# Kernel tuning notes

Measured on AMD Instinct MI355X. Metric: run time of the kernel, lower is better.

## Reference

```python
import jax, jax.numpy as jnp
import numpy as np

GAMMA = 0.01
INFER_STEP = 3


def softor(x, axis, gamma=GAMMA):
    # smoothed logic-OR: gamma*logsumexp(x/gamma), normalized if it exceeds 1 (alphailp/NSFR semantics)
    lse = gamma * jax.nn.logsumexp(x / gamma, axis=axis)
    m = jnp.max(lse)
    return jnp.where(m > 1.0, lse / m, lse)


def clause_eval(R, I, gamma=GAMMA):
    # R: [C,B,G] per-clause valuations, I: [C,G,S,L] index tensor (values in [0,G))
    # gathered[c,b,g,s,l] = R[c, b, I[c,g,s,l]]
    gathered = jax.vmap(lambda Rc, Ic: jnp.take(Rc, Ic, axis=1))(R, I)  # [C,B,G,S,L]
    body = jnp.prod(gathered, axis=-1)  # product over body atoms L -> [C,B,G,S]
    return softor(body, axis=-1, gamma=gamma)  # soft-OR over substitutions S -> [C,B,G]


def setup_inputs() -> dict:
    key = jax.random.key(0)
    k1, k2 = jax.random.split(key)
    C, B, G, S, L = 4, 128, 2048, 32, 3
    x = jax.random.uniform(k1, (B, G), dtype=jnp.float32)  # atom valuations in [0,1]
    I = jax.random.randint(k2, (C, G, S, L), 0, G, dtype=jnp.int32)
    return {"x": x, "I": I}


def reference(x, I):
    C = I.shape[0]
    B, G = x.shape
    R = jnp.broadcast_to(x[None], (C, B, G))  # expand to per-clause valuation
    for _ in range(INFER_STEP):
        # amalgamate previous valuation with one inference step via soft-OR along stacked dim
        R = softor(jnp.stack([R, clause_eval(R, I)], axis=1), axis=1)
    return R
```

## Files before the change

### kernel.cpp

```cpp
#include <hip/hip_runtime.h>
#include <cstdint>
#include <cstddef>

#define C_ 4
#define B_ 128
#define G_ 2048
#define S_ 32
#define L_ 3
#define NSTEP_ 3
#define GAMMA_ 0.01f
#define INVG_LOG2E_ 144.26950408889634f
#define GAMMA_LN2_ 0.0069314718055994530942f

__device__ __forceinline__ float slot_max(const uint32_t* slots, int slot) {
  float m = 0.0f;
#pragma unroll
  for (int k = 0; k < 8; ++k)
    m = fmaxf(m, __uint_as_float(slots[slot * 128 + k * 16]));
  return m;
}

__global__ __launch_bounds__(256) void k_init(const float* __restrict__ x,
                                              float* __restrict__ A) {
  __shared__ float tile[32][33];
  const int g0 = blockIdx.x * 32, b0 = blockIdx.y * 32, c = blockIdx.z;
  const int tx = threadIdx.x;
  for (int i = threadIdx.y; i < 32; i += 8)
    tile[i][tx] = x[(size_t)(b0 + i) * G_ + g0 + tx];
  __syncthreads();
  for (int j = threadIdx.y; j < 32; j += 8)
    A[((size_t)c * G_ + g0 + j) * B_ + b0 + tx] = tile[tx][j];
}

__global__ __launch_bounds__(128) void k_gather(const float* __restrict__ A,
                                                const int* __restrict__ Idx,
                                                float* __restrict__ Lout,
                                                uint32_t* slots,
                                                int prev_slot, int out_slot) {
  __shared__ int sidx[S_ * L_];
  __shared__ float wmax[2];
  const int tid = threadIdx.x;
  const int bid = blockIdx.x;
  const int cg = ((bid & 7) << 10) | (bid >> 3);
  const int c = cg >> 11;

  if (tid < S_ * L_) sidx[tid] = Idx[(size_t)cg * (S_ * L_) + tid];
  const float mprev = slot_max(slots, prev_slot);
  const float scale = (mprev > 1.0f) ? (1.0f / mprev) : 1.0f;
  const float s3 = scale * scale * scale;
  __syncthreads();

  const float* Ac = A + (size_t)c * (G_ * B_) + tid;
  float body[S_];
#pragma unroll
  for (int s = 0; s < S_; ++s) {
    const float v0 = Ac[(size_t)sidx[3 * s + 0] * B_];
    const float v1 = Ac[(size_t)sidx[3 * s + 1] * B_];
    const float v2 = Ac[(size_t)sidx[3 * s + 2] * B_];
    body[s] = v0 * v1 * v2;
  }
  float m = body[0];
#pragma unroll
  for (int s = 1; s < S_; ++s) m = fmaxf(m, body[s]);
  const float K = s3 * INVG_LOG2E_;
  float acc = 0.0f;
#pragma unroll
  for (int s = 0; s < S_; ++s) acc += exp2f((body[s] - m) * K);
  const float lse = m * s3 + GAMMA_LN2_ * log2f(acc);
  Lout[(size_t)cg * B_ + tid] = lse;

  float t = lse;
#pragma unroll
  for (int off = 32; off >= 1; off >>= 1) t = fmaxf(t, __shfl_xor(t, off));
  if ((tid & 63) == 0) wmax[tid >> 6] = t;
  __syncthreads();
  if (tid == 0)
    atomicMax(slots + out_slot * 128 + (bid & 7) * 16,
              __float_as_uint(fmaxf(wmax[0], wmax[1])));
}

__global__ __launch_bounds__(256) void k_elem(float* __restrict__ A,
                                              const float* __restrict__ Lin,
                                              uint32_t* slots,
                                              int prev_slot, int m1_slot,
                                              int out_slot) {
  __shared__ float wmax[4];
  const float mprev = slot_max(slots, prev_slot);
  const float sprev = (mprev > 1.0f) ? (1.0f / mprev) : 1.0f;
  const float m1 = slot_max(slots, m1_slot);
  const float s1 = (m1 > 1.0f) ? (1.0f / m1) : 1.0f;

  const int e = (blockIdx.x * 256 + threadIdx.x) * 4;
  const float4 Rv = *reinterpret_cast<const float4*>(A + e);
  const float4 Lv = *reinterpret_cast<const float4*>(Lin + e);

  float r[4] = {Rv.x, Rv.y, Rv.z, Rv.w};
  float l[4] = {Lv.x, Lv.y, Lv.z, Lv.w};
  float o[4];
  float tmax = 0.0f;
#pragma unroll
  for (int k = 0; k < 4; ++k) {
    const float R = r[k] * sprev;
    const float ce = l[k] * s1;
    const float M = fmaxf(R, ce);
    const float mn = fminf(R, ce);
    const float lse2 =
        M + GAMMA_LN2_ * log2f(1.0f + exp2f((mn - M) * INVG_LOG2E_));
    o[k] = lse2;
    tmax = fmaxf(tmax, lse2);
  }
  *reinterpret_cast<float4*>(A + e) = make_float4(o[0], o[1], o[2], o[3]);

  float t = tmax;
#pragma unroll
  for (int off = 32; off >= 1; off >>= 1) t = fmaxf(t, __shfl_xor(t, off));
  if ((threadIdx.x & 63) == 0) wmax[threadIdx.x >> 6] = t;
  __syncthreads();
  if (threadIdx.x == 0) {
    const float bm =
        fmaxf(fmaxf(wmax[0], wmax[1]), fmaxf(wmax[2], wmax[3]));
    atomicMax(slots + out_slot * 128 + (blockIdx.x & 7) * 16,
              __float_as_uint(bm));
  }
}

__global__ __launch_bounds__(256) void k_out(const float* __restrict__ A,
                                             float* __restrict__ out,
                                             const uint32_t* __restrict__ slots,
                                             int mslot) {
  __shared__ float tile[32][33];
  const float mfin = slot_max(slots, mslot);
  const float sc = (mfin > 1.0f) ? (1.0f / mfin) : 1.0f;
  const int g0 = blockIdx.x * 32, b0 = blockIdx.y * 32, c = blockIdx.z;
  const int tx = threadIdx.x;
  for (int j = threadIdx.y; j < 32; j += 8)
    tile[j][tx] = A[((size_t)c * G_ + g0 + j) * B_ + b0 + tx];
  __syncthreads();
  for (int i = threadIdx.y; i < 32; i += 8)
    out[((size_t)c * B_ + b0 + i) * G_ + g0 + tx] = tile[tx][i] * sc;
}

extern "C" void kernel_launch(void* const* d_in, const int* in_sizes, int n_in,
                              void* d_out, int out_size, void* d_ws,
                              size_t ws_size, hipStream_t stream) {
  const float* x = (const float*)d_in[0];
  const int* Idx = (const int*)d_in[1];
  float* out = (float*)d_out;

  char* ws = (char*)d_ws;
  uint32_t* slots = (uint32_t*)ws;
  float* A = (float*)(ws + 4096);
  float* Lb = (float*)(ws + 4096 + (size_t)C_ * G_ * B_ * 4);

  hipMemsetAsync(slots, 0, 4096, stream);

  dim3 tb(32, 8);
  k_init<<<dim3(G_ / 32, B_ / 32, C_), tb, 0, stream>>>(x, A);

  for (int step = 0; step < NSTEP_; ++step) {
    const int prev = 2 * step;
    const int m1s = 2 * step + 1;
    const int m2s = 2 * step + 2;
    k_gather<<<C_ * G_, 128, 0, stream>>>(A, Idx, Lb, slots, prev, m1s);
    k_elem<<<(C_ * G_ * B_) / (256 * 4), 256, 0, stream>>>(A, Lb, slots, prev,
                                                           m1s, m2s);
  }

  k_out<<<dim3(G_ / 32, B_ / 32, C_), tb, 0, stream>>>(A, out, slots,
                                                       2 * NSTEP_);
}
```

Measured before the change: 163.2 us.

## Use single-wave gather with online logsumexp and shared transposed input for first step

The gather kernel now runs one 64-lane wave per (clause, atom) row. Each lane handles two batch elements with float2 loads and reads indices through readfirstlane scalar loads, dropping the shared-memory staging and the block barrier. The 32-element body array is replaced by an online max/logsumexp recurrence, which trades register pressure for extra exp2 work. The init kernel also writes one transposed copy of x instead of four per-clause copies, and step 0 reads that copy with a zero clause stride, cutting init writes and improving cache hits on the first gather.

Result: slower. 243.9 us (+49.4%).

```diff
diff --git a/kernel.cpp b/kernel.cpp
--- a/kernel.cpp
+++ b/kernel.cpp
@@ -20,70 +20,69 @@
   return m;
 }
 
-__global__ __launch_bounds__(256) void k_init(const float* __restrict__ x,
-                                              float* __restrict__ A) {
+__global__ __launch_bounds__(256) void k_initT(const float* __restrict__ x,
+                                               float* __restrict__ xT) {
   __shared__ float tile[32][33];
-  const int g0 = blockIdx.x * 32, b0 = blockIdx.y * 32, c = blockIdx.z;
+  const int g0 = blockIdx.x * 32, b0 = blockIdx.y * 32;
   const int tx = threadIdx.x;
   for (int i = threadIdx.y; i < 32; i += 8)
     tile[i][tx] = x[(size_t)(b0 + i) * G_ + g0 + tx];
   __syncthreads();
   for (int j = threadIdx.y; j < 32; j += 8)
-    A[((size_t)c * G_ + g0 + j) * B_ + b0 + tx] = tile[tx][j];
+    xT[(size_t)(g0 + j) * B_ + b0 + tx] = tile[tx][j];
 }
 
-__global__ __launch_bounds__(128) void k_gather(const float* __restrict__ A,
-                                                const int* __restrict__ Idx,
-                                                float* __restrict__ Lout,
-                                                uint32_t* slots,
-                                                int prev_slot, int out_slot) {
-  __shared__ int sidx[S_ * L_];
-  __shared__ float wmax[2];
-  const int tid = threadIdx.x;
+__global__ __launch_bounds__(64, 4) void k_gather(
+    const float* __restrict__ Abase, size_t cstride,
+    const int* __restrict__ Idx, float* __restrict__ Lout,
+    uint32_t* slots, int prev_slot, int out_slot) {
+  const int lane = threadIdx.x;
   const int bid = blockIdx.x;
   const int cg = ((bid & 7) << 10) | (bid >> 3);
   const int c = cg >> 11;
 
-  if (tid < S_ * L_) sidx[tid] = Idx[(size_t)cg * (S_ * L_) + tid];
   const float mprev = slot_max(slots, prev_slot);
   const float scale = (mprev > 1.0f) ? (1.0f / mprev) : 1.0f;
   const float s3 = scale * scale * scale;
-  __syncthreads();
+  const float K = s3 * INVG_LOG2E_;
 
-  const float* Ac = A + (size_t)c * (G_ * B_) + tid;
-  float body[S_];
+  const int ibase = cg * (S_ * L_);
+  const float* Ac = Abase + (size_t)c * cstride + 2 * lane;
+
+  float M0 = -1.0f, M1 = -1.0f;
+  float acc0 = 0.0f, acc1 = 0.0f;
 #pragma unroll
   for (int s = 0; s < S_; ++s) {
-    const float v0 = Ac[(size_t)sidx[3 * s + 0] * B_];
-    const float v1 = Ac[(size_t)sidx[3 * s + 1] * B_];
-    const float v2 = Ac[(size_t)sidx[3 * s + 2] * B_];
-    body[s] = v0 * v1 * v2;
+    const int r0 = __builtin_amdgcn_readfirstlane(Idx[ibase + 3 * s + 0]);
+    const int r1 = __builtin_amdgcn_readfirstlane(Idx[ibase + 3 * s + 1]);
+    const int r2 = __builtin_amdgcn_readfirstlane(Idx[ibase + 3 * s + 2]);
+    const float2 v0 = *(const float2*)(Ac + (size_t)r0 * B_);
+    const float2 v1 = *(const float2*)(Ac + (size_t)r1 * B_);
+    const float2 v2 = *(const float2*)(Ac + (size_t)r2 * B_);
+    const float b0 = v0.x * v1.x * v2.x;
+    const float b1 = v0.y * v1.y * v2.y;
+    const float n0 = fmaxf(M0, b0);
+    acc0 = acc0 * exp2f((M0 - n0) * K) + exp2f((b0 - n0) * K);
+    M0 = n0;
+    const float n1 = fmaxf(M1, b1);
+    acc1 = acc1 * exp2f((M1 - n1) * K) + exp2f((b1 - n1) * K);
+    M1 = n1;
   }
-  float m = body[0];
-#pragma unroll
-  for (int s = 1; s < S_; ++s) m = fmaxf(m, body[s]);
-  const float K = s3 * INVG_LOG2E_;
-  float acc = 0.0f;
-#pragma unroll
-  for (int s = 0; s < S_; ++s) acc += exp2f((body[s] - m) * K);
-  const float lse = m * s3 + GAMMA_LN2_ * log2f(acc);
-  Lout[(size_t)cg * B_ + tid] = lse;
+  const float lse0 = M0 * s3 + GAMMA_LN2_ * log2f(acc0);
+  const float lse1 = M1 * s3 + GAMMA_LN2_ * log2f(acc1);
+  *(float2*)(Lout + (size_t)cg * B_ + 2 * lane) = make_float2(lse0, lse1);
 
-  float t = lse;
+  float t = fmaxf(lse0, lse1);
 #pragma unroll
   for (int off = 32; off >= 1; off >>= 1) t = fmaxf(t, __shfl_xor(t, off));
-  if ((tid & 63) == 0) wmax[tid >> 6] = t;
-  __syncthreads();
-  if (tid == 0)
-    atomicMax(slots + out_slot * 128 + (bid & 7) * 16,
-              __float_as_uint(fmaxf(wmax[0], wmax[1])));
+  if (lane == 0)
+    atomicMax(slots + out_slot * 128 + (bid & 7) * 16, __float_as_uint(t));
 }
 
-__global__ __launch_bounds__(256) void k_elem(float* __restrict__ A,
-                                              const float* __restrict__ Lin,
-                                              uint32_t* slots,
-                                              int prev_slot, int m1_slot,
-                                              int out_slot) {
+__global__ __launch_bounds__(256) void k_elem(
+    const float* __restrict__ Rin, size_t rstride, float* __restrict__ A,
+    const float* __restrict__ Lin, uint32_t* slots, int prev_slot,
+    int m1_slot, int out_slot) {
   __shared__ float wmax[4];
   const float mprev = slot_max(slots, prev_slot);
   const float sprev = (mprev > 1.0f) ? (1.0f / mprev) : 1.0f;
@@ -91,7 +90,9 @@
   const float s1 = (m1 > 1.0f) ? (1.0f / m1) : 1.0f;
 
   const int e = (blockIdx.x * 256 + threadIdx.x) * 4;
-  const float4 Rv = *reinterpret_cast<const float4*>(A + e);
+  const int c = e >> 18;
+  const int rem = e & (G_ * B_ - 1);
+  const float4 Rv = *reinterpret_cast<const float4*>(Rin + (size_t)c * rstride + rem);
   const float4 Lv = *reinterpret_cast<const float4*>(Lin + e);
 
   float r[4] = {Rv.x, Rv.y, Rv.z, Rv.w};
@@ -117,8 +118,7 @@
   if ((threadIdx.x & 63) == 0) wmax[threadIdx.x >> 6] = t;
   __syncthreads();
   if (threadIdx.x == 0) {
-    const float bm =
-        fmaxf(fmaxf(wmax[0], wmax[1]), fmaxf(wmax[2], wmax[3]));
+    const float bm = fmaxf(fmaxf(wmax[0], wmax[1]), fmaxf(wmax[2], wmax[3]));
     atomicMax(slots + out_slot * 128 + (blockIdx.x & 7) * 16,
               __float_as_uint(bm));
   }
@@ -151,21 +151,25 @@
   uint32_t* slots = (uint32_t*)ws;
   float* A = (float*)(ws + 4096);
   float* Lb = (float*)(ws + 4096 + (size_t)C_ * G_ * B_ * 4);
+  float* xT = (float*)(ws + 4096 + (size_t)C_ * G_ * B_ * 8);
 
   hipMemsetAsync(slots, 0, 4096, stream);
 
-  dim3 tb(32, 8);
-  k_init<<<dim3(G_ / 32, B_ / 32, C_), tb, 0, stream>>>(x, A);
+  k_initT<<<dim3(G_ / 32, B_ / 32), dim3(32, 8), 0, stream>>>(x, xT);
 
+  const size_t CS = (size_t)G_ * B_;
   for (int step = 0; step < NSTEP_; ++step) {
     const int prev = 2 * step;
     const int m1s = 2 * step + 1;
     const int m2s = 2 * step + 2;
-    k_gather<<<C_ * G_, 128, 0, stream>>>(A, Idx, Lb, slots, prev, m1s);
-    k_elem<<<(C_ * G_ * B_) / (256 * 4), 256, 0, stream>>>(A, Lb, slots, prev,
-                                                           m1s, m2s);
+    const float* Rsrc = (step == 0) ? xT : A;
+    const size_t rs = (step == 0) ? 0 : CS;
+    k_gather<<<C_ * G_, 64, 0, stream>>>(Rsrc, rs, Idx, Lb, slots, prev, m1s);
+    k_elem<<<(C_ * G_ * B_) / (256 * 4), 256, 0, stream>>>(Rsrc, rs, A, Lb,
+                                                           slots, prev, m1s,
+                                                           m2s);
   }
 
-  k_out<<<dim3(G_ / 32, B_ / 32, C_), tb, 0, stream>>>(A, out, slots,
-                                                       2 * NSTEP_);
+  k_out<<<dim3(G_ / 32, B_ / 32, C_), dim3(32, 8), 0, stream>>>(A, out, slots,
+                                                                2 * NSTEP_);
 }
```
